# Performance work log

Measured on AMD Instinct MI355X. Metric: run time of the kernel, lower is better.

## Reference

```python
import jax, jax.numpy as jnp
import numpy as np

DIM = 1024

def setup_inputs() -> dict:
    key = jax.random.key(0)
    k1, k2, k3, k4 = jax.random.split(key, 4)
    x = jax.random.normal(k1, (8, 2048, DIM), dtype=jnp.float32)
    # torch Linear weights: y = x @ W.T
    w_qkv = jax.random.normal(k2, (3 * DIM, DIM), dtype=jnp.float32) * (DIM ** -0.5)
    w_proj = jax.random.normal(k3, (DIM, DIM), dtype=jnp.float32) * (DIM ** -0.5)
    b_proj = jax.random.normal(k4, (DIM,), dtype=jnp.float32) * 0.01
    return {"x": x, "w_qkv": w_qkv, "w_proj": w_proj, "b_proj": b_proj}

def reference(x, w_qkv, w_proj, b_proj):
    B, N, C = x.shape
    scale = C ** -0.5
    qkv = jnp.einsum('bnc,dc->bnd', x, w_qkv).reshape(B, N, 3, C)
    q, k, v = qkv[:, :, 0], qkv[:, :, 1], qkv[:, :, 2]  # each [B,N,C]
    attn = jnp.einsum('bnc,bmc->bnm', q, k) * scale      # [B,N,N]
    attn = jax.nn.softmax(attn, axis=-1)
    o = jnp.einsum('bnm,bmc->bnc', attn, v)              # [B,N,C]
    # faithful to torch: (attn@v).transpose(1,2).reshape(B,N,C) permutes data
    o = jnp.swapaxes(o, 1, 2).reshape(B, N, C)
    return jnp.einsum('bnc,dc->bnd', o, w_proj) + b_proj
```

## Files before the change

kernel.cpp:

```cpp
#include <hip/hip_runtime.h>

typedef __bf16 bf16x8_t __attribute__((ext_vector_type(8)));
typedef float f32x4_t __attribute__((ext_vector_type(4)));

#define AS1 __attribute__((address_space(1)))
#define AS3 __attribute__((address_space(3)))

__device__ __forceinline__ unsigned short f2b(float f) {
    unsigned u = __builtin_bit_cast(unsigned, f);
    u += 0x7fffu + ((u >> 16) & 1u);
    return (unsigned short)(u >> 16);
}
__device__ __forceinline__ float b2f(unsigned short s) {
    return __builtin_bit_cast(float, (unsigned)s << 16);
}

__global__ __launch_bounds__(256) void k_f2b(const float* __restrict__ in,
                                             unsigned short* __restrict__ out,
                                             int n4) {
    int i = blockIdx.x * 256 + threadIdx.x;
    if (i >= n4) return;
    float4 v = reinterpret_cast<const float4*>(in)[i];
    ushort4 o;
    o.x = f2b(v.x); o.y = f2b(v.y); o.z = f2b(v.z); o.w = f2b(v.w);
    reinterpret_cast<ushort4*>(out)[i] = o;
}

#define STA(h, i)                                                              \
    __builtin_amdgcn_global_load_lds(                                         \
        (const AS1 void*)(pA + kof + (size_t)((h) * 128 + (i) * 8) * lda),    \
        (AS3 void*)(wb + (h) * 16384 + wave * 2048 + (i) * 1024), 16, 0, 0)
#define STB(h, i)                                                              \
    __builtin_amdgcn_global_load_lds(                                         \
        (const AS1 void*)(pB + kof + (size_t)((h) * 128 + (i) * 8) * ldb),    \
        (AS3 void*)(wb + 32768 + (h) * 16384 + wave * 2048 + (i) * 1024), 16, 0, 0)

#define READ_A(qm)                                                             \
    _Pragma("unroll") for (int mi = 0; mi < 4; ++mi)                           \
        _Pragma("unroll") for (int ks = 0; ks < 2; ++ks)                       \
            af[mi][ks] = *reinterpret_cast<const bf16x8_t*>(rb + offA[qm][mi][ks]);
#define READ_B(qn)                                                             \
    _Pragma("unroll") for (int ni = 0; ni < 2; ++ni)                           \
        _Pragma("unroll") for (int ks = 0; ks < 2; ++ks)                       \
            bf[qn][ni][ks] = *reinterpret_cast<const bf16x8_t*>(rb + offB[qn][ni][ks]);

#define MFMA_QUAD(qm, qn)                                                      \
    __builtin_amdgcn_s_setprio(1);                                             \
    _Pragma("unroll") for (int mi = 0; mi < 4; ++mi)                           \
        _Pragma("unroll") for (int ni = 0; ni < 2; ++ni) {                     \
            acc[qm][qn][mi][ni] = __builtin_amdgcn_mfma_f32_16x16x32_bf16(     \
                af[mi][0], bf[qn][ni][0], acc[qm][qn][mi][ni], 0, 0, 0);       \
            acc[qm][qn][mi][ni] = __builtin_amdgcn_mfma_f32_16x16x32_bf16(     \
                af[mi][1], bf[qn][ni][1], acc[qm][qn][mi][ni], 0, 0, 0);       \
        }                                                                      \
    __builtin_amdgcn_s_setprio(0);

template <bool LAST>
__device__ __forceinline__ void tile_step(
    const char* rb, char* wb, size_t kof,
    const unsigned short* pA, const unsigned short* pB, int lda, int ldb,
    int wave, const int offA[2][4][2], const int offB[2][2][2],
    f32x4_t acc[2][2][4][2]) {
    bf16x8_t af[4][2], bf[2][2][2];
    asm volatile("s_waitcnt vmcnt(2)" ::: "memory");
    asm volatile("s_barrier" ::: "memory");
    if constexpr (!LAST) { STA(0, 0); STA(0, 1); STB(0, 0); STB(0, 1); }
    READ_A(0); READ_B(0); READ_B(1);
    MFMA_QUAD(0, 0);
    MFMA_QUAD(0, 1);
    if constexpr (LAST) asm volatile("s_waitcnt vmcnt(0)" ::: "memory");
    else                asm volatile("s_waitcnt vmcnt(4)" ::: "memory");
    asm volatile("s_barrier" ::: "memory");
    if constexpr (!LAST) { STB(1, 0); STB(1, 1); STA(1, 0); STA(1, 1); }
    READ_A(1);
    MFMA_QUAD(1, 1);
    MFMA_QUAD(1, 0);
}

__device__ __forceinline__ void gemm_mainloop(
    const unsigned short* __restrict__ A, int lda,
    const unsigned short* __restrict__ B, int ldb,
    int K, char* smem, f32x4_t acc[2][2][4][2]) {
    const int tid = threadIdx.x;
    const int wave = tid >> 6, lane = tid & 63;
    const int wsm = (wave >> 2) & 1, wsn = wave & 3;
    const int fr = lane & 15, g = lane >> 4;
    const int srow8 = lane >> 3;
    const int scolB = ((lane & 7) * 16) ^ (srow8 << 4);

    const unsigned short* pA = A + (size_t)(wave * 16 + srow8) * lda + (scolB >> 1);
    const unsigned short* pB = B + (size_t)(wave * 16 + srow8) * ldb + (scolB >> 1);

    int offA[2][4][2], offB[2][2][2];
#pragma unroll
    for (int qm = 0; qm < 2; ++qm)
#pragma unroll
        for (int mi = 0; mi < 4; ++mi)
#pragma unroll
            for (int ks = 0; ks < 2; ++ks)
                offA[qm][mi][ks] = qm * 16384 + (wsm * 64 + mi * 16 + fr) * 128 +
                                   ((ks * 64 + g * 16) ^ ((fr & 7) << 4));
#pragma unroll
    for (int qn = 0; qn < 2; ++qn)
#pragma unroll
        for (int ni = 0; ni < 2; ++ni)
#pragma unroll
            for (int ks = 0; ks < 2; ++ks)
                offB[qn][ni][ks] = 32768 + qn * 16384 + (wsn * 32 + ni * 16 + fr) * 128 +
                                   ((ks * 64 + g * 16) ^ ((fr & 7) << 4));

#pragma unroll
    for (int qm = 0; qm < 2; ++qm)
#pragma unroll
        for (int qn = 0; qn < 2; ++qn)
#pragma unroll
            for (int mi = 0; mi < 4; ++mi)
#pragma unroll
                for (int ni = 0; ni < 2; ++ni)
                    acc[qm][qn][mi][ni] = (f32x4_t){0.f, 0.f, 0.f, 0.f};

    const int NT = K >> 6;

    {
        char* wb = smem;
        const size_t kof = 0;
        STA(0, 0); STA(0, 1);
        STB(0, 0); STB(0, 1);
        STB(1, 0); STB(1, 1);
        STA(1, 0); STA(1, 1);
    }

    for (int t = 0; t < NT - 1; ++t) {
        const char* rb = smem + (size_t)(t & 1) * 65536;
        char* wb = smem + (size_t)((t & 1) ^ 1) * 65536;
        tile_step<false>(rb, wb, (size_t)(t + 1) * 64, pA, pB, lda, ldb,
                         wave, offA, offB, acc);
    }
    {
        const char* rb = smem + (size_t)((NT - 1) & 1) * 65536;
        tile_step<true>(rb, smem, 0, pA, pB, lda, ldb, wave, offA, offB, acc);
    }
}

#define EPILOGUE_IDX                                            \
    const int lane = threadIdx.x & 63, wave = threadIdx.x >> 6; \
    const int e_r0 = ((wave >> 2) & 1) * 64 + (lane >> 4) * 4;  \
    const int e_c0 = (wave & 3) * 32 + (lane & 15);

#define EPILOGUE_LOOP(...)                                      \
    _Pragma("unroll") for (int qm = 0; qm < 2; ++qm)            \
    _Pragma("unroll") for (int qn = 0; qn < 2; ++qn)            \
    _Pragma("unroll") for (int mi = 0; mi < 4; ++mi)            \
    _Pragma("unroll") for (int ni = 0; ni < 2; ++ni)            \
    _Pragma("unroll") for (int j = 0; j < 4; ++j) { __VA_ARGS__ }


__global__ __launch_bounds__(512, 2) void k_gemm_qkv_qk(
    const unsigned short* __restrict__ x, const unsigned short* __restrict__ w,
    unsigned short* __restrict__ qk) {
    __shared__ __align__(16) char smem[131072];
    const size_t tm = (size_t)blockIdx.x * 256, tn = (size_t)blockIdx.y * 256;
    f32x4_t acc[2][2][4][2];
    gemm_mainloop(x + tm * 1024, 1024, w + tn * 1024, 1024, 1024, smem, acc);
    EPILOGUE_IDX
    EPILOGUE_LOOP(
        size_t m = tm + qm * 128 + e_r0 + mi * 16 + j;
        size_t z = m >> 11;
        size_t nloc = m & 2047;
        int n = (int)tn + qn * 128 + e_c0 + ni * 16;
        unsigned short v = f2b(acc[qm][qn][mi][ni][j]);
        size_t base = z * 4194304 + nloc * 1024;
        if (n < 1024) qk[base + n] = v;
        else          qk[base + 2097152 + (n - 1024)] = v;
    )
}

__global__ __launch_bounds__(512, 2) void k_gemm_vt(
    const unsigned short* __restrict__ wv, const unsigned short* __restrict__ x,
    unsigned short* __restrict__ vt) {
    __shared__ __align__(16) char smem[131072];
    const size_t tm = (size_t)blockIdx.x * 256, tn = (size_t)blockIdx.y * 256;
    f32x4_t acc[2][2][4][2];
    gemm_mainloop(wv + tm * 1024, 1024, x + tn * 1024, 1024, 1024, smem, acc);
    EPILOGUE_IDX
    EPILOGUE_LOOP(
        size_t m = tm + qm * 128 + e_r0 + mi * 16 + j;
        size_t n = tn + qn * 128 + e_c0 + ni * 16;
        vt[m * 16384 + n] = f2b(acc[qm][qn][mi][ni][j]);
    )
}

__global__ __launch_bounds__(512, 2) void k_gemm_scores(
    const unsigned short* __restrict__ qk, unsigned short* __restrict__ S, int z0) {
    __shared__ __align__(16) char smem[131072];
    const size_t z = z0 + blockIdx.z;
    const size_t tm = (size_t)blockIdx.x * 256, tn = (size_t)blockIdx.y * 256;
    const unsigned short* qz = qk + z * 4194304;
    const unsigned short* kz = qz + 2097152;
    f32x4_t acc[2][2][4][2];
    gemm_mainloop(qz + tm * 1024, 1024, kz + tn * 1024, 1024, 1024, smem, acc);
    EPILOGUE_IDX
    unsigned short* Sz = S + (size_t)blockIdx.z * 4194304;
    EPILOGUE_LOOP(
        size_t m = tm + qm * 128 + e_r0 + mi * 16 + j;
        size_t n = tn + qn * 128 + e_c0 + ni * 16;
        Sz[m * 2048 + n] = f2b(acc[qm][qn][mi][ni][j] * 0.03125f);
    )
}

__global__ __launch_bounds__(256) void k_softmax(const unsigned short* __restrict__ S,
                                                 unsigned short* __restrict__ qk,
                                                 int z0) {
    const size_t r = blockIdx.x;
    const int t = threadIdx.x, wv = t >> 6, ln = t & 63;
    const uint4 u = reinterpret_cast<const uint4*>(S + r * 2048)[t];
    float vals[8];
    vals[0] = b2f((unsigned short)(u.x & 0xffff)); vals[1] = b2f((unsigned short)(u.x >> 16));
    vals[2] = b2f((unsigned short)(u.y & 0xffff)); vals[3] = b2f((unsigned short)(u.y >> 16));
    vals[4] = b2f((unsigned short)(u.z & 0xffff)); vals[5] = b2f((unsigned short)(u.z >> 16));
    vals[6] = b2f((unsigned short)(u.w & 0xffff)); vals[7] = b2f((unsigned short)(u.w >> 16));

    float mx = vals[0];
#pragma unroll
    for (int i = 1; i < 8; ++i) mx = fmaxf(mx, vals[i]);
#pragma unroll
    for (int i = 32; i > 0; i >>= 1) mx = fmaxf(mx, __shfl_xor(mx, i, 64));
    __shared__ float red[8];
    if (ln == 0) red[wv] = mx;
    __syncthreads();
    mx = fmaxf(fmaxf(red[0], red[1]), fmaxf(red[2], red[3]));

    float ex[8], s = 0.f;
#pragma unroll
    for (int i = 0; i < 8; ++i) { ex[i] = __expf(vals[i] - mx); s += ex[i]; }
#pragma unroll
    for (int i = 32; i > 0; i >>= 1) s += __shfl_xor(s, i, 64);
    if (ln == 0) red[4 + wv] = s;
    __syncthreads();
    s = (red[4] + red[5]) + (red[6] + red[7]);
    float inv = 1.0f / s;

    uint4 o;
    o.x = (unsigned)f2b(ex[0] * inv) | ((unsigned)f2b(ex[1] * inv) << 16);
    o.y = (unsigned)f2b(ex[2] * inv) | ((unsigned)f2b(ex[3] * inv) << 16);
    o.z = (unsigned)f2b(ex[4] * inv) | ((unsigned)f2b(ex[5] * inv) << 16);
    o.w = (unsigned)f2b(ex[6] * inv) | ((unsigned)f2b(ex[7] * inv) << 16);

    const size_t zg = z0 + (r >> 11), nloc = r & 2047;
    reinterpret_cast<uint4*>(qk + zg * 4194304 + nloc * 2048)[t] = o;
}

__global__ __launch_bounds__(512, 2) void k_gemm_pv(
    const unsigned short* __restrict__ vt, const unsigned short* __restrict__ qk,
    unsigned short* __restrict__ ob, int z0) {
    __shared__ __align__(16) char smem[131072];
    const size_t z = z0 + blockIdx.z;
    const size_t tm = (size_t)blockIdx.x * 256, tn = (size_t)blockIdx.y * 256;
    const unsigned short* P = qk + z * 4194304;
    f32x4_t acc[2][2][4][2];
    gemm_mainloop(vt + tm * 16384 + z * 2048, 16384,
                  P + tn * 2048, 2048, 2048, smem, acc);
    EPILOGUE_IDX
    unsigned short* oz = ob + z * 2097152;
    EPILOGUE_LOOP(
        size_t m = tm + qm * 128 + e_r0 + mi * 16 + j;
        size_t n = tn + qn * 128 + e_c0 + ni * 16;
        oz[(2 * m + (n >> 10)) * 1024 + (n & 1023)] = f2b(acc[qm][qn][mi][ni][j]);
    )
}

__global__ __launch_bounds__(512, 2) void k_gemm_proj(
    const unsigned short* __restrict__ o2, const unsigned short* __restrict__ w,
    const float* __restrict__ bias, float* __restrict__ out) {
    __shared__ __align__(16) char smem[131072];
    const size_t tm = (size_t)blockIdx.x * 256, tn = (size_t)blockIdx.y * 256;
    f32x4_t acc[2][2][4][2];
    gemm_mainloop(o2 + tm * 1024, 1024, w + tn * 1024, 1024, 1024, smem, acc);
    EPILOGUE_IDX
    EPILOGUE_LOOP(
        size_t m = tm + qm * 128 + e_r0 + mi * 16 + j;
        size_t n = tn + qn * 128 + e_c0 + ni * 16;
        out[m * 1024 + n] = acc[qm][qn][mi][ni][j] + bias[n];
    )
}

extern "C" void kernel_launch(void* const* d_in, const int* in_sizes, int n_in,
                              void* d_out, int out_size, void* d_ws, size_t ws_size,
                              hipStream_t stream) {
    const float* x     = (const float*)d_in[0];
    const float* wqkv  = (const float*)d_in[1];
    const float* wproj = (const float*)d_in[2];
    const float* bproj = (const float*)d_in[3];
    float* out = (float*)d_out;
    char* ws = (char*)d_ws;

    const size_t off_xb    = 0;
    const size_t off_wqkv  = 33554432;
    const size_t off_wproj = 39845888;
    const size_t off_qk    = 41943040;
    const size_t off_vt    = 109051904;
    const size_t off_S     = 142606336;
    int NZ = 0;
    for (int c = 8; c >= 1; c >>= 1)
        if (off_S + (size_t)c * 8388608 <= ws_size) { NZ = c; break; }
    if (NZ == 0) return;

    unsigned short* xb     = (unsigned short*)(ws + off_xb);
    unsigned short* wqkvb  = (unsigned short*)(ws + off_wqkv);
    unsigned short* wprojb = (unsigned short*)(ws + off_wproj);
    unsigned short* qkb    = (unsigned short*)(ws + off_qk);
    unsigned short* vtb    = (unsigned short*)(ws + off_vt);
    unsigned short* Sb     = (unsigned short*)(ws + off_S);
    unsigned short* obuf   = (unsigned short*)(ws + off_xb);

    k_f2b<<<16384, 256, 0, stream>>>(x, xb, 4194304);
    k_f2b<<<3072, 256, 0, stream>>>(wqkv, wqkvb, 786432);
    k_f2b<<<1024, 256, 0, stream>>>(wproj, wprojb, 262144);

    k_gemm_qkv_qk<<<dim3(64, 8), 512, 0, stream>>>(xb, wqkvb, qkb);
    k_gemm_vt<<<dim3(4, 64), 512, 0, stream>>>(wqkvb + (size_t)2048 * 1024, xb, vtb);

    for (int z0 = 0; z0 < 8; z0 += NZ) {
        k_gemm_scores<<<dim3(8, 8, NZ), 512, 0, stream>>>(qkb, Sb, z0);
        k_softmax<<<NZ * 2048, 256, 0, stream>>>(Sb, qkb, z0);
        k_gemm_pv<<<dim3(4, 8, NZ), 512, 0, stream>>>(vtb, qkb, obuf, z0);
    }
    k_gemm_proj<<<dim3(64, 4), 512, 0, stream>>>(obuf, wprojb, bproj, out);
}
```

Measured before the change: 328.8 us.

## Switch GEMMs to 256x128 tiles with K=32 triple-buffered LDS pipeline

Replaces the shared GEMM mainloop: the block tile shrinks from 256x256 to 256x128, the K step from 64 to 32, and the LDS double buffer becomes a three-stage ring of 24KB stages without XOR swizzle. Launch bounds move to 4 blocks per CU and the grids double in N. The aim is more resident blocks and better latency hiding. In exchange, operand reuse per block drops, global traffic rises, and the unswizzled LDS reads may hit bank conflicts.

```diff
diff --git a/kernel.cpp b/kernel.cpp
--- a/kernel.cpp
+++ b/kernel.cpp
@@ -26,185 +26,139 @@
     reinterpret_cast<ushort4*>(out)[i] = o;
 }
 
-#define STA(h, i)                                                              \
-    __builtin_amdgcn_global_load_lds(                                         \
-        (const AS1 void*)(pA + kof + (size_t)((h) * 128 + (i) * 8) * lda),    \
-        (AS3 void*)(wb + (h) * 16384 + wave * 2048 + (i) * 1024), 16, 0, 0)
-#define STB(h, i)                                                              \
-    __builtin_amdgcn_global_load_lds(                                         \
-        (const AS1 void*)(pB + kof + (size_t)((h) * 128 + (i) * 8) * ldb),    \
-        (AS3 void*)(wb + 32768 + (h) * 16384 + wave * 2048 + (i) * 1024), 16, 0, 0)
-
-#define READ_A(qm)                                                             \
-    _Pragma("unroll") for (int mi = 0; mi < 4; ++mi)                           \
-        _Pragma("unroll") for (int ks = 0; ks < 2; ++ks)                       \
-            af[mi][ks] = *reinterpret_cast<const bf16x8_t*>(rb + offA[qm][mi][ks]);
-#define READ_B(qn)                                                             \
-    _Pragma("unroll") for (int ni = 0; ni < 2; ++ni)                           \
-        _Pragma("unroll") for (int ks = 0; ks < 2; ++ks)                       \
-            bf[qn][ni][ks] = *reinterpret_cast<const bf16x8_t*>(rb + offB[qn][ni][ks]);
-
-#define MFMA_QUAD(qm, qn)                                                      \
-    __builtin_amdgcn_s_setprio(1);                                             \
-    _Pragma("unroll") for (int mi = 0; mi < 4; ++mi)                           \
-        _Pragma("unroll") for (int ni = 0; ni < 2; ++ni) {                     \
-            acc[qm][qn][mi][ni] = __builtin_amdgcn_mfma_f32_16x16x32_bf16(     \
-                af[mi][0], bf[qn][ni][0], acc[qm][qn][mi][ni], 0, 0, 0);       \
-            acc[qm][qn][mi][ni] = __builtin_amdgcn_mfma_f32_16x16x32_bf16(     \
-                af[mi][1], bf[qn][ni][1], acc[qm][qn][mi][ni], 0, 0, 0);       \
-        }                                                                      \
-    __builtin_amdgcn_s_setprio(0);
-
-template <bool LAST>
-__device__ __forceinline__ void tile_step(
-    const char* rb, char* wb, size_t kof,
-    const unsigned short* pA, const unsigned short* pB, int lda, int ldb,
-    int wave, const int offA[2][4][2], const int offB[2][2][2],
-    f32x4_t acc[2][2][4][2]) {
-    bf16x8_t af[4][2], bf[2][2][2];
-    asm volatile("s_waitcnt vmcnt(2)" ::: "memory");
-    asm volatile("s_barrier" ::: "memory");
-    if constexpr (!LAST) { STA(0, 0); STA(0, 1); STB(0, 0); STB(0, 1); }
-    READ_A(0); READ_B(0); READ_B(1);
-    MFMA_QUAD(0, 0);
-    MFMA_QUAD(0, 1);
-    if constexpr (LAST) asm volatile("s_waitcnt vmcnt(0)" ::: "memory");
-    else                asm volatile("s_waitcnt vmcnt(4)" ::: "memory");
-    asm volatile("s_barrier" ::: "memory");
-    if constexpr (!LAST) { STB(1, 0); STB(1, 1); STA(1, 0); STA(1, 1); }
-    READ_A(1);
-    MFMA_QUAD(1, 1);
-    MFMA_QUAD(1, 0);
-}
+#define STAGE(tt, bb) do {                                                     \
+    char* dst_ = smem + (bb) * 24576;                                          \
+    const size_t kof_ = (size_t)(tt) * 32;                                     \
+    __builtin_amdgcn_global_load_lds((const AS1 void*)(pA0 + kof_),            \
+        (AS3 void*)(dst_ + wave * 1024), 16, 0, 0);                            \
+    __builtin_amdgcn_global_load_lds((const AS1 void*)(pA1 + kof_),            \
+        (AS3 void*)(dst_ + 8192 + wave * 1024), 16, 0, 0);                     \
+    __builtin_amdgcn_global_load_lds((const AS1 void*)(pB0 + kof_),            \
+        (AS3 void*)(dst_ + 16384 + wave * 1024), 16, 0, 0);                    \
+} while (0)
 
 __device__ __forceinline__ void gemm_mainloop(
     const unsigned short* __restrict__ A, int lda,
     const unsigned short* __restrict__ B, int ldb,
-    int K, char* smem, f32x4_t acc[2][2][4][2]) {
+    int K, char* smem, f32x4_t acc[4][4]) {
     const int tid = threadIdx.x;
     const int wave = tid >> 6, lane = tid & 63;
-    const int wsm = (wave >> 2) & 1, wsn = wave & 3;
+    const int wm = wave >> 1, wn = wave & 1;
     const int fr = lane & 15, g = lane >> 4;
-    const int srow8 = lane >> 3;
-    const int scolB = ((lane & 7) * 16) ^ (srow8 << 4);
-
-    const unsigned short* pA = A + (size_t)(wave * 16 + srow8) * lda + (scolB >> 1);
-    const unsigned short* pB = B + (size_t)(wave * 16 + srow8) * ldb + (scolB >> 1);
-
-    int offA[2][4][2], offB[2][2][2];
-#pragma unroll
-    for (int qm = 0; qm < 2; ++qm)
+
+    const unsigned short* pA0 = A + (size_t)(wave * 16 + (lane >> 2)) * lda + (lane & 3) * 8;
+    const unsigned short* pA1 = pA0 + (size_t)128 * lda;
+    const unsigned short* pB0 = B + (size_t)(wave * 16 + (lane >> 2)) * ldb + (lane & 3) * 8;
+
+    int offA[4], offB[4];
+#pragma unroll
+    for (int mi = 0; mi < 4; ++mi)
+        offA[mi] = (wm * 64 + mi * 16 + fr) * 64 + g * 16;
+#pragma unroll
+    for (int ni = 0; ni < 4; ++ni)
+        offB[ni] = 16384 + (wn * 64 + ni * 16 + fr) * 64 + g * 16;
+
+#pragma unroll
+    for (int mi = 0; mi < 4; ++mi)
+#pragma unroll
+        for (int ni = 0; ni < 4; ++ni)
+            acc[mi][ni] = (f32x4_t){0.f, 0.f, 0.f, 0.f};
+
+    const int NT = K >> 5;
+
+    STAGE(0, 0);
+    STAGE(1, 1);
+
+    int cb = 0;
+    for (int t = 0; t < NT; ++t) {
+        if (t + 1 < NT) asm volatile("s_waitcnt vmcnt(3)" ::: "memory");
+        else            asm volatile("s_waitcnt vmcnt(0)" ::: "memory");
+        asm volatile("s_barrier" ::: "memory");
+        if (t + 2 < NT) {
+            int sb = cb + 2; if (sb >= 3) sb -= 3;
+            STAGE(t + 2, sb);
+        }
+        const char* rb = smem + cb * 24576;
+        bf16x8_t af[4], bfv[4];
 #pragma unroll
         for (int mi = 0; mi < 4; ++mi)
-#pragma unroll
-            for (int ks = 0; ks < 2; ++ks)
-                offA[qm][mi][ks] = qm * 16384 + (wsm * 64 + mi * 16 + fr) * 128 +
-                                   ((ks * 64 + g * 16) ^ ((fr & 7) << 4));
-#pragma unroll
-    for (int qn = 0; qn < 2; ++qn)
-#pragma unroll
-        for (int ni = 0; ni < 2; ++ni)
-#pragma unroll
-            for (int ks = 0; ks < 2; ++ks)
-                offB[qn][ni][ks] = 32768 + qn * 16384 + (wsn * 32 + ni * 16 + fr) * 128 +
-                                   ((ks * 64 + g * 16) ^ ((fr & 7) << 4));
-
-#pragma unroll
-    for (int qm = 0; qm < 2; ++qm)
-#pragma unroll
-        for (int qn = 0; qn < 2; ++qn)
-#pragma unroll
-            for (int mi = 0; mi < 4; ++mi)
-#pragma unroll
-                for (int ni = 0; ni < 2; ++ni)
-                    acc[qm][qn][mi][ni] = (f32x4_t){0.f, 0.f, 0.f, 0.f};
-
-    const int NT = K >> 6;
-
-    {
-        char* wb = smem;
-        const size_t kof = 0;
-        STA(0, 0); STA(0, 1);
-        STB(0, 0); STB(0, 1);
-        STB(1, 0); STB(1, 1);
-        STA(1, 0); STA(1, 1);
-    }
-
-    for (int t = 0; t < NT - 1; ++t) {
-        const char* rb = smem + (size_t)(t & 1) * 65536;
-        char* wb = smem + (size_t)((t & 1) ^ 1) * 65536;
-        tile_step<false>(rb, wb, (size_t)(t + 1) * 64, pA, pB, lda, ldb,
-                         wave, offA, offB, acc);
-    }
-    {
-        const char* rb = smem + (size_t)((NT - 1) & 1) * 65536;
-        tile_step<true>(rb, smem, 0, pA, pB, lda, ldb, wave, offA, offB, acc);
+            af[mi] = *reinterpret_cast<const bf16x8_t*>(rb + offA[mi]);
+#pragma unroll
+        for (int ni = 0; ni < 4; ++ni)
+            bfv[ni] = *reinterpret_cast<const bf16x8_t*>(rb + offB[ni]);
+        __builtin_amdgcn_s_setprio(1);
+#pragma unroll
+        for (int mi = 0; mi < 4; ++mi)
+#pragma unroll
+            for (int ni = 0; ni < 4; ++ni)
+                acc[mi][ni] = __builtin_amdgcn_mfma_f32_16x16x32_bf16(
+                    af[mi], bfv[ni], acc[mi][ni], 0, 0, 0);
+        __builtin_amdgcn_s_setprio(0);
+        cb = (cb + 1 == 3) ? 0 : cb + 1;
     }
 }
 
 #define EPILOGUE_IDX                                            \
     const int lane = threadIdx.x & 63, wave = threadIdx.x >> 6; \
-    const int e_r0 = ((wave >> 2) & 1) * 64 + (lane >> 4) * 4;  \
-    const int e_c0 = (wave & 3) * 32 + (lane & 15);
+    const int e_r0 = (wave >> 1) * 64 + (lane >> 4) * 4;        \
+    const int e_c0 = (wave & 1) * 64 + (lane & 15);
 
 #define EPILOGUE_LOOP(...)                                      \
-    _Pragma("unroll") for (int qm = 0; qm < 2; ++qm)            \
-    _Pragma("unroll") for (int qn = 0; qn < 2; ++qn)            \
     _Pragma("unroll") for (int mi = 0; mi < 4; ++mi)            \
-    _Pragma("unroll") for (int ni = 0; ni < 2; ++ni)            \
+    _Pragma("unroll") for (int ni = 0; ni < 4; ++ni)            \
     _Pragma("unroll") for (int j = 0; j < 4; ++j) { __VA_ARGS__ }
 
 
-__global__ __launch_bounds__(512, 2) void k_gemm_qkv_qk(
+__global__ __launch_bounds__(512, 4) void k_gemm_qkv_qk(
     const unsigned short* __restrict__ x, const unsigned short* __restrict__ w,
     unsigned short* __restrict__ qk) {
-    __shared__ __align__(16) char smem[131072];
-    const size_t tm = (size_t)blockIdx.x * 256, tn = (size_t)blockIdx.y * 256;
-    f32x4_t acc[2][2][4][2];
+    __shared__ __align__(16) char smem[73728];
+    const size_t tm = (size_t)blockIdx.x * 256, tn = (size_t)blockIdx.y * 128;
+    f32x4_t acc[4][4];
     gemm_mainloop(x + tm * 1024, 1024, w + tn * 1024, 1024, 1024, smem, acc);
     EPILOGUE_IDX
     EPILOGUE_LOOP(
-        size_t m = tm + qm * 128 + e_r0 + mi * 16 + j;
+        size_t m = tm + e_r0 + mi * 16 + j;
         size_t z = m >> 11;
         size_t nloc = m & 2047;
-        int n = (int)tn + qn * 128 + e_c0 + ni * 16;
-        unsigned short v = f2b(acc[qm][qn][mi][ni][j]);
+        int n = (int)tn + e_c0 + ni * 16;
+        unsigned short v = f2b(acc[mi][ni][j]);
         size_t base = z * 4194304 + nloc * 1024;
         if (n < 1024) qk[base + n] = v;
         else          qk[base + 2097152 + (n - 1024)] = v;
     )
 }
 
-__global__ __launch_bounds__(512, 2) void k_gemm_vt(
+__global__ __launch_bounds__(512, 4) void k_gemm_vt(
     const unsigned short* __restrict__ wv, const unsigned short* __restrict__ x,
     unsigned short* __restrict__ vt) {
-    __shared__ __align__(16) char smem[131072];
-    const size_t tm = (size_t)blockIdx.x * 256, tn = (size_t)blockIdx.y * 256;
-    f32x4_t acc[2][2][4][2];
+    __shared__ __align__(16) char smem[73728];
+    const size_t tm = (size_t)blockIdx.x * 256, tn = (size_t)blockIdx.y * 128;
+    f32x4_t acc[4][4];
     gemm_mainloop(wv + tm * 1024, 1024, x + tn * 1024, 1024, 1024, smem, acc);
     EPILOGUE_IDX
     EPILOGUE_LOOP(
-        size_t m = tm + qm * 128 + e_r0 + mi * 16 + j;
-        size_t n = tn + qn * 128 + e_c0 + ni * 16;
-        vt[m * 16384 + n] = f2b(acc[qm][qn][mi][ni][j]);
-    )
-}
-
-__global__ __launch_bounds__(512, 2) void k_gemm_scores(
+        size_t m = tm + e_r0 + mi * 16 + j;
+        size_t n = tn + e_c0 + ni * 16;
+        vt[m * 16384 + n] = f2b(acc[mi][ni][j]);
+    )
+}
+
+__global__ __launch_bounds__(512, 4) void k_gemm_scores(
     const unsigned short* __restrict__ qk, unsigned short* __restrict__ S, int z0) {
-    __shared__ __align__(16) char smem[131072];
+    __shared__ __align__(16) char smem[73728];
     const size_t z = z0 + blockIdx.z;
-    const size_t tm = (size_t)blockIdx.x * 256, tn = (size_t)blockIdx.y * 256;
+    const size_t tm = (size_t)blockIdx.x * 256, tn = (size_t)blockIdx.y * 128;
     const unsigned short* qz = qk + z * 4194304;
     const unsigned short* kz = qz + 2097152;
-    f32x4_t acc[2][2][4][2];
+    f32x4_t acc[4][4];
     gemm_mainloop(qz + tm * 1024, 1024, kz + tn * 1024, 1024, 1024, smem, acc);
     EPILOGUE_IDX
     unsigned short* Sz = S + (size_t)blockIdx.z * 4194304;
     EPILOGUE_LOOP(
-        size_t m = tm + qm * 128 + e_r0 + mi * 16 + j;
-        size_t n = tn + qn * 128 + e_c0 + ni * 16;
-        Sz[m * 2048 + n] = f2b(acc[qm][qn][mi][ni][j] * 0.03125f);
+        size_t m = tm + e_r0 + mi * 16 + j;
+        size_t n = tn + e_c0 + ni * 16;
+        Sz[m * 2048 + n] = f2b(acc[mi][ni][j] * 0.03125f);
     )
 }
 
@@ -250,37 +204,37 @@
     reinterpret_cast<uint4*>(qk + zg * 4194304 + nloc * 2048)[t] = o;
 }
 
-__global__ __launch_bounds__(512, 2) void k_gemm_pv(
+__global__ __launch_bounds__(512, 4) void k_gemm_pv(
     const unsigned short* __restrict__ vt, const unsigned short* __restrict__ qk,
     unsigned short* __restrict__ ob, int z0) {
-    __shared__ __align__(16) char smem[131072];
+    __shared__ __align__(16) char smem[73728];
     const size_t z = z0 + blockIdx.z;
-    const size_t tm = (size_t)blockIdx.x * 256, tn = (size_t)blockIdx.y * 256;
+    const size_t tm = (size_t)blockIdx.x * 256, tn = (size_t)blockIdx.y * 128;
     const unsigned short* P = qk + z * 4194304;
-    f32x4_t acc[2][2][4][2];
+    f32x4_t acc[4][4];
     gemm_mainloop(vt + tm * 16384 + z * 2048, 16384,
                   P + tn * 2048, 2048, 2048, smem, acc);
     EPILOGUE_IDX
     unsigned short* oz = ob + z * 2097152;
     EPILOGUE_LOOP(
-        size_t m = tm + qm * 128 + e_r0 + mi * 16 + j;
-        size_t n = tn + qn * 128 + e_c0 + ni * 16;
-        oz[(2 * m + (n >> 10)) * 1024 + (n & 1023)] = f2b(acc[qm][qn][mi][ni][j]);
-    )
-}
-
-__global__ __launch_bounds__(512, 2) void k_gemm_proj(
+        size_t m = tm + e_r0 + mi * 16 + j;
+        size_t n = tn + e_c0 + ni * 16;
+        oz[(2 * m + (n >> 10)) * 1024 + (n & 1023)] = f2b(acc[mi][ni][j]);
+    )
+}
+
+__global__ __launch_bounds__(512, 4) void k_gemm_proj(
     const unsigned short* __restrict__ o2, const unsigned short* __restrict__ w,
     const float* __restrict__ bias, float* __restrict__ out) {
-    __shared__ __align__(16) char smem[131072];
-    const size_t tm = (size_t)blockIdx.x * 256, tn = (size_t)blockIdx.y * 256;
-    f32x4_t acc[2][2][4][2];
+    __shared__ __align__(16) char smem[73728];
+    const size_t tm = (size_t)blockIdx.x * 256, tn = (size_t)blockIdx.y * 128;
+    f32x4_t acc[4][4];
     gemm_mainloop(o2 + tm * 1024, 1024, w + tn * 1024, 1024, 1024, smem, acc);
     EPILOGUE_IDX
     EPILOGUE_LOOP(
-        size_t m = tm + qm * 128 + e_r0 + mi * 16 + j;
-        size_t n = tn + qn * 128 + e_c0 + ni * 16;
-        out[m * 1024 + n] = acc[qm][qn][mi][ni][j] + bias[n];
+        size_t m = tm + e_r0 + mi * 16 + j;
+        size_t n = tn + e_c0 + ni * 16;
+        out[m * 1024 + n] = acc[mi][ni][j] + bias[n];
     )
 }
 
@@ -317,13 +271,13 @@
     k_f2b<<<3072, 256, 0, stream>>>(wqkv, wqkvb, 786432);
     k_f2b<<<1024, 256, 0, stream>>>(wproj, wprojb, 262144);
 
-    k_gemm_qkv_qk<<<dim3(64, 8), 512, 0, stream>>>(xb, wqkvb, qkb);
-    k_gemm_vt<<<dim3(4, 64), 512, 0, stream>>>(wqkvb + (size_t)2048 * 1024, xb, vtb);
+    k_gemm_qkv_qk<<<dim3(64, 16), 512, 0, stream>>>(xb, wqkvb, qkb);
+    k_gemm_vt<<<dim3(4, 128), 512, 0, stream>>>(wqkvb + (size_t)2048 * 1024, xb, vtb);
 
     for (int z0 = 0; z0 < 8; z0 += NZ) {
-        k_gemm_scores<<<dim3(8, 8, NZ), 512, 0, stream>>>(qkb, Sb, z0);
+        k_gemm_scores<<<dim3(8, 16, NZ), 512, 0, stream>>>(qkb, Sb, z0);
         k_softmax<<<NZ * 2048, 256, 0, stream>>>(Sb, qkb, z0);
-        k_gemm_pv<<<dim3(4, 8, NZ), 512, 0, stream>>>(vtb, qkb, obuf, z0);
+        k_gemm_pv<<<dim3(4, 16, NZ), 512, 0, stream>>>(vtb, qkb, obuf, z0);
     }
-    k_gemm_proj<<<dim3(64, 4), 512, 0, stream>>>(obuf, wprojb, bproj, out);
-}
+    k_gemm_proj<<<dim3(64, 8), 512, 0, stream>>>(obuf, wprojb, bproj, out);
+}
```

Measured after the change: 368.7 us. +12.1%, slower.

## Add 256x128 triple-buffered GEMM mainloop for QKV and V^T projections

Applied to the files above, without the earlier changes.

Introduces a new GEMM mainloop with a 256x128 output tile, K-step of 32, and a three-stage LDS ring of 24 KB per stage, used by the QKV and V^T projection kernels in place of the 256x256 double-buffered loop. These kernels now use about 72 KB of shared memory, launch bounds of (512, 4) and twice as many blocks, aiming for better occupancy, more grid parallelism and deeper prefetch. The trade-off is less operand reuse per tile and a per-thread register cap under the new launch bounds. The scores, PV and output-projection kernels keep the original mainloop.

```diff
diff --git a/kernel.cpp b/kernel.cpp
--- a/kernel.cpp
+++ b/kernel.cpp
@@ -25,6 +25,90 @@
     o.x = f2b(v.x); o.y = f2b(v.y); o.z = f2b(v.z); o.w = f2b(v.w);
     reinterpret_cast<ushort4*>(out)[i] = o;
 }
+
+#define STAGE3(tt, bb) do {                                                    \
+    char* dst_ = smem + (bb) * 24576;                                          \
+    const size_t kof_ = (size_t)(tt) * 32;                                     \
+    __builtin_amdgcn_global_load_lds((const AS1 void*)(pA0 + kof_),            \
+        (AS3 void*)(dst_ + wave * 1024), 16, 0, 0);                            \
+    __builtin_amdgcn_global_load_lds((const AS1 void*)(pA1 + kof_),            \
+        (AS3 void*)(dst_ + 8192 + wave * 1024), 16, 0, 0);                     \
+    __builtin_amdgcn_global_load_lds((const AS1 void*)(pB0 + kof_),            \
+        (AS3 void*)(dst_ + 16384 + wave * 1024), 16, 0, 0);                    \
+} while (0)
+
+__device__ __forceinline__ void gemm_ml_128(
+    const unsigned short* __restrict__ A, int lda,
+    const unsigned short* __restrict__ B, int ldb,
+    int K, char* smem, f32x4_t acc[4][4]) {
+    const int tid = threadIdx.x;
+    const int wave = tid >> 6, lane = tid & 63;
+    const int wm = wave >> 1, wn = wave & 1;
+    const int fr = lane & 15, g = lane >> 4;
+
+    const int scolB = ((lane & 3) * 16) ^ (((lane >> 3) & 3) << 4);
+    const unsigned short* pA0 = A + (size_t)(wave * 16 + (lane >> 2)) * lda + (scolB >> 1);
+    const unsigned short* pA1 = pA0 + (size_t)128 * lda;
+    const unsigned short* pB0 = B + (size_t)(wave * 16 + (lane >> 2)) * ldb + (scolB >> 1);
+
+    const int rswz = (g * 16) ^ (((fr >> 1) & 3) << 4);
+    int offA[4], offB[4];
+#pragma unroll
+    for (int mi = 0; mi < 4; ++mi)
+        offA[mi] = (wm * 64 + mi * 16 + fr) * 64 + rswz;
+#pragma unroll
+    for (int ni = 0; ni < 4; ++ni)
+        offB[ni] = 16384 + (wn * 64 + ni * 16 + fr) * 64 + rswz;
+
+#pragma unroll
+    for (int mi = 0; mi < 4; ++mi)
+#pragma unroll
+        for (int ni = 0; ni < 4; ++ni)
+            acc[mi][ni] = (f32x4_t){0.f, 0.f, 0.f, 0.f};
+
+    const int NT = K >> 5;
+
+    STAGE3(0, 0);
+    STAGE3(1, 1);
+
+    int cb = 0;
+    for (int t = 0; t < NT; ++t) {
+        if (t + 1 < NT) asm volatile("s_waitcnt vmcnt(3)" ::: "memory");
+        else            asm volatile("s_waitcnt vmcnt(0)" ::: "memory");
+        asm volatile("s_barrier" ::: "memory");
+        if (t + 2 < NT) {
+            int sb = cb + 2; if (sb >= 3) sb -= 3;
+            STAGE3(t + 2, sb);
+        }
+        const char* rb = smem + cb * 24576;
+        bf16x8_t af[4], bfv[4];
+#pragma unroll
+        for (int mi = 0; mi < 4; ++mi)
+            af[mi] = *reinterpret_cast<const bf16x8_t*>(rb + offA[mi]);
+#pragma unroll
+        for (int ni = 0; ni < 4; ++ni)
+            bfv[ni] = *reinterpret_cast<const bf16x8_t*>(rb + offB[ni]);
+        __builtin_amdgcn_s_setprio(1);
+#pragma unroll
+        for (int mi = 0; mi < 4; ++mi)
+#pragma unroll
+            for (int ni = 0; ni < 4; ++ni)
+                acc[mi][ni] = __builtin_amdgcn_mfma_f32_16x16x32_bf16(
+                    af[mi], bfv[ni], acc[mi][ni], 0, 0, 0);
+        __builtin_amdgcn_s_setprio(0);
+        cb = (cb + 1 == 3) ? 0 : cb + 1;
+    }
+}
+
+#define E128_IDX                                                \
+    const int lane = threadIdx.x & 63, wave = threadIdx.x >> 6; \
+    const int e_r0 = (wave >> 1) * 64 + (lane >> 4) * 4;        \
+    const int e_c0 = (wave & 1) * 64 + (lane & 15);
+
+#define E128_LOOP(...)                                          \
+    _Pragma("unroll") for (int mi = 0; mi < 4; ++mi)            \
+    _Pragma("unroll") for (int ni = 0; ni < 4; ++ni)            \
+    _Pragma("unroll") for (int j = 0; j < 4; ++j) { __VA_ARGS__ }
 
 #define STA(h, i)                                                              \
     __builtin_amdgcn_global_load_lds(                                         \
@@ -77,7 +161,7 @@
     MFMA_QUAD(1, 0);
 }
 
-__device__ __forceinline__ void gemm_mainloop(
+__device__ __forceinline__ void gemm_ml_256(
     const unsigned short* __restrict__ A, int lda,
     const unsigned short* __restrict__ B, int ldb,
     int K, char* smem, f32x4_t acc[2][2][4][2]) {
@@ -142,12 +226,12 @@
     }
 }
 
-#define EPILOGUE_IDX                                            \
+#define E256_IDX                                                \
     const int lane = threadIdx.x & 63, wave = threadIdx.x >> 6; \
     const int e_r0 = ((wave >> 2) & 1) * 64 + (lane >> 4) * 4;  \
     const int e_c0 = (wave & 3) * 32 + (lane & 15);
 
-#define EPILOGUE_LOOP(...)                                      \
+#define E256_LOOP(...)                                          \
     _Pragma("unroll") for (int qm = 0; qm < 2; ++qm)            \
     _Pragma("unroll") for (int qn = 0; qn < 2; ++qn)            \
     _Pragma("unroll") for (int mi = 0; mi < 4; ++mi)            \
@@ -155,38 +239,38 @@
     _Pragma("unroll") for (int j = 0; j < 4; ++j) { __VA_ARGS__ }
 
 
-__global__ __launch_bounds__(512, 2) void k_gemm_qkv_qk(
+__global__ __launch_bounds__(512, 4) void k_gemm_qkv_qk(
     const unsigned short* __restrict__ x, const unsigned short* __restrict__ w,
     unsigned short* __restrict__ qk) {
-    __shared__ __align__(16) char smem[131072];
-    const size_t tm = (size_t)blockIdx.x * 256, tn = (size_t)blockIdx.y * 256;
-    f32x4_t acc[2][2][4][2];
-    gemm_mainloop(x + tm * 1024, 1024, w + tn * 1024, 1024, 1024, smem, acc);
-    EPILOGUE_IDX
-    EPILOGUE_LOOP(
-        size_t m = tm + qm * 128 + e_r0 + mi * 16 + j;
+    __shared__ __align__(16) char smem[73728];
+    const size_t tm = (size_t)blockIdx.x * 256, tn = (size_t)blockIdx.y * 128;
+    f32x4_t acc[4][4];
+    gemm_ml_128(x + tm * 1024, 1024, w + tn * 1024, 1024, 1024, smem, acc);
+    E128_IDX
+    E128_LOOP(
+        size_t m = tm + e_r0 + mi * 16 + j;
         size_t z = m >> 11;
         size_t nloc = m & 2047;
-        int n = (int)tn + qn * 128 + e_c0 + ni * 16;
-        unsigned short v = f2b(acc[qm][qn][mi][ni][j]);
+        int n = (int)tn + e_c0 + ni * 16;
+        unsigned short v = f2b(acc[mi][ni][j]);
         size_t base = z * 4194304 + nloc * 1024;
         if (n < 1024) qk[base + n] = v;
         else          qk[base + 2097152 + (n - 1024)] = v;
     )
 }
 
-__global__ __launch_bounds__(512, 2) void k_gemm_vt(
+__global__ __launch_bounds__(512, 4) void k_gemm_vt(
     const unsigned short* __restrict__ wv, const unsigned short* __restrict__ x,
     unsigned short* __restrict__ vt) {
-    __shared__ __align__(16) char smem[131072];
-    const size_t tm = (size_t)blockIdx.x * 256, tn = (size_t)blockIdx.y * 256;
-    f32x4_t acc[2][2][4][2];
-    gemm_mainloop(wv + tm * 1024, 1024, x + tn * 1024, 1024, 1024, smem, acc);
-    EPILOGUE_IDX
-    EPILOGUE_LOOP(
-        size_t m = tm + qm * 128 + e_r0 + mi * 16 + j;
-        size_t n = tn + qn * 128 + e_c0 + ni * 16;
-        vt[m * 16384 + n] = f2b(acc[qm][qn][mi][ni][j]);
+    __shared__ __align__(16) char smem[73728];
+    const size_t tm = (size_t)blockIdx.x * 256, tn = (size_t)blockIdx.y * 128;
+    f32x4_t acc[4][4];
+    gemm_ml_128(wv + tm * 1024, 1024, x + tn * 1024, 1024, 1024, smem, acc);
+    E128_IDX
+    E128_LOOP(
+        size_t m = tm + e_r0 + mi * 16 + j;
+        size_t n = tn + e_c0 + ni * 16;
+        vt[m * 16384 + n] = f2b(acc[mi][ni][j]);
     )
 }
 
@@ -198,10 +282,10 @@
     const unsigned short* qz = qk + z * 4194304;
     const unsigned short* kz = qz + 2097152;
     f32x4_t acc[2][2][4][2];
-    gemm_mainloop(qz + tm * 1024, 1024, kz + tn * 1024, 1024, 1024, smem, acc);
-    EPILOGUE_IDX
+    gemm_ml_256(qz + tm * 1024, 1024, kz + tn * 1024, 1024, 1024, smem, acc);
+    E256_IDX
     unsigned short* Sz = S + (size_t)blockIdx.z * 4194304;
-    EPILOGUE_LOOP(
+    E256_LOOP(
         size_t m = tm + qm * 128 + e_r0 + mi * 16 + j;
         size_t n = tn + qn * 128 + e_c0 + ni * 16;
         Sz[m * 2048 + n] = f2b(acc[qm][qn][mi][ni][j] * 0.03125f);
@@ -258,11 +342,11 @@
     const size_t tm = (size_t)blockIdx.x * 256, tn = (size_t)blockIdx.y * 256;
     const unsigned short* P = qk + z * 4194304;
     f32x4_t acc[2][2][4][2];
-    gemm_mainloop(vt + tm * 16384 + z * 2048, 16384,
-                  P + tn * 2048, 2048, 2048, smem, acc);
-    EPILOGUE_IDX
+    gemm_ml_256(vt + tm * 16384 + z * 2048, 16384,
+                P + tn * 2048, 2048, 2048, smem, acc);
+    E256_IDX
     unsigned short* oz = ob + z * 2097152;
-    EPILOGUE_LOOP(
+    E256_LOOP(
         size_t m = tm + qm * 128 + e_r0 + mi * 16 + j;
         size_t n = tn + qn * 128 + e_c0 + ni * 16;
         oz[(2 * m + (n >> 10)) * 1024 + (n & 1023)] = f2b(acc[qm][qn][mi][ni][j]);
@@ -275,9 +359,9 @@
     __shared__ __align__(16) char smem[131072];
     const size_t tm = (size_t)blockIdx.x * 256, tn = (size_t)blockIdx.y * 256;
     f32x4_t acc[2][2][4][2];
-    gemm_mainloop(o2 + tm * 1024, 1024, w + tn * 1024, 1024, 1024, smem, acc);
-    EPILOGUE_IDX
-    EPILOGUE_LOOP(
+    gemm_ml_256(o2 + tm * 1024, 1024, w + tn * 1024, 1024, 1024, smem, acc);
+    E256_IDX
+    E256_LOOP(
         size_t m = tm + qm * 128 + e_r0 + mi * 16 + j;
         size_t n = tn + qn * 128 + e_c0 + ni * 16;
         out[m * 1024 + n] = acc[qm][qn][mi][ni][j] + bias[n];
@@ -317,8 +401,8 @@
     k_f2b<<<3072, 256, 0, stream>>>(wqkv, wqkvb, 786432);
     k_f2b<<<1024, 256, 0, stream>>>(wproj, wprojb, 262144);
 
-    k_gemm_qkv_qk<<<dim3(64, 8), 512, 0, stream>>>(xb, wqkvb, qkb);
-    k_gemm_vt<<<dim3(4, 64), 512, 0, stream>>>(wqkvb + (size_t)2048 * 1024, xb, vtb);
+    k_gemm_qkv_qk<<<dim3(64, 16), 512, 0, stream>>>(xb, wqkvb, qkb);
+    k_gemm_vt<<<dim3(4, 128), 512, 0, stream>>>(wqkvb + (size_t)2048 * 1024, xb, vtb);
 
     for (int z0 = 0; z0 < 8; z0 += NZ) {
         k_gemm_scores<<<dim3(8, 8, NZ), 512, 0, stream>>>(qkb, Sb, z0);
```

Measured after the change: 341.1 us. +3.7%, slower.
